# Optimization experiments

Measured on AMD Instinct MI355X. Metric: run time of the kernel, lower is better.

## Reference

```python
import jax, jax.numpy as jnp
import numpy as np

THRESH = 1.0
# Control points exactly as in the source (including the [5.0, 1.0] literal).
SRC = np.array([[0.0, 0.0], [0.5, 0.0], [1.0, 0.0],
                [0.0, 0.5], [0.5, 0.5], [1.0, 0.5],
                [0.0, 1.0], [5.0, 1.0], [1.0, 1.0]], dtype=np.float32)


def _u(r):
    # TPS radial basis: r^2 * log(r + 1e-6)
    return r * r * jnp.log(r + 1e-6)


def _pd(a, b):
    # pairwise euclidean distance a:[M,2], b:[N,2] -> [M,N]
    return jnp.sqrt(jnp.sum((a[:, None, :] - b[None, :, :]) ** 2, -1))


def _tps_fit(c, v):
    # Solve TPS system for control points c:[n,2] with target values v:[n].
    # Returns 'reduced' theta of length n+2 (drops theta[0]), as in tps_theta_from_points(reduced=True).
    n = c.shape[0]
    U = _u(_pd(c, c))                                      # [n,n]
    P = jnp.concatenate([jnp.ones((n, 1), c.dtype), c], 1)  # [n,3]
    A = jnp.zeros((n + 3, n + 3), c.dtype)
    A = A.at[:n, :n].set(U).at[:n, n:].set(P).at[n:, :n].set(P.T)
    rhs = jnp.concatenate([v, jnp.zeros((3,), c.dtype)])
    theta = jnp.linalg.solve(A, rhs)
    return theta[1:]


def _tps_z(x, c, theta):
    # Evaluate reduced TPS at points x:[M,2] with control points c:[n,2].
    w, a = theta[:-3], theta[-3:]
    w = jnp.concatenate([-jnp.sum(w, keepdims=True), w])   # recover dropped weight
    b = _u(_pd(x, c)) @ w                                  # [M]
    return a[0] + a[1] * x[:, 0] + a[2] * x[:, 1] + b


def _tps_grid(mv, H, W):
    # mv:[9,2] moving vectors -> warp grid [H,W,2] in [0,1] coords (x in ch 0, y in ch 1)
    src = jnp.asarray(SRC)
    dst = src + mv
    delta = src - dst                                       # = -mv, as in tps_theta_from_points
    th_x = _tps_fit(dst, delta[:, 0])
    th_y = _tps_fit(dst, delta[:, 1])
    ug = jnp.stack(jnp.meshgrid(jnp.linspace(0.0, 1.0, W, dtype=jnp.float32),
                                jnp.linspace(0.0, 1.0, H, dtype=jnp.float32)), -1)  # [H,W,2]
    xf = ug.reshape(-1, 2)
    dx = _tps_z(xf, dst, th_x).reshape(H, W)
    dy = _tps_z(xf, dst, th_y).reshape(H, W)
    return jnp.stack([dx, dy], -1) + ug


def setup_inputs() -> dict:
    key = jax.random.key(0)
    k1, k2 = jax.random.split(key)
    geo_parameters = jax.random.normal(k1, (8, 9, 2), dtype=jnp.float32) * 0.05
    corr_scores = jax.random.uniform(k2, (8, 48, 48, 48, 48), dtype=jnp.float32)
    return {"geo_parameters": geo_parameters, "corr_scores": corr_scores}


def reference(geo_parameters, corr_scores):
    B = corr_scores.shape[0]
    H, W = corr_scores.shape[-2], corr_scores.shape[-1]
    grids = jax.vmap(lambda mv: _tps_grid(mv, H, W))(geo_parameters)  # [B,H,W,2]
    # Faithful to source: grid * (height-1, width-1) scales channel 0 (x) by H-1, channel 1 (y) by W-1.
    gx = grids[..., 0] * (H - 1)
    gy = grids[..., 1] * (W - 1)
    ax = jnp.arange(W, dtype=gx.dtype)
    ay = jnp.arange(H, dtype=gy.dtype)
    # integer ax in [ceil(gx-t), floor(gx+t)] (clipped to valid range) <=> |ax-gx| <= t
    cx = jnp.abs(ax[None, :, None, None] - gx[:, None, :, :]) <= THRESH  # [B,W_a,H_b,W_b]
    cy = jnp.abs(ay[None, :, None, None] - gy[:, None, :, :]) <= THRESH  # [B,H_a,H_b,W_b]
    mask = (cy[:, :, None, :, :] & cx[:, None, :, :, :]).astype(corr_scores.dtype)  # [B,H,W,H,W]
    inlier_matching = corr_scores * mask
    return inlier_matching, jnp.sum(inlier_matching, axis=(1, 2, 3, 4))
```

## Files before the change

kernel.cpp:

```cpp
#include <hip/hip_runtime.h>

#define HW 48
#define GRID_PER_B (HW * HW)
#define CORR_PER_B (HW * HW * HW * HW)

typedef float f32x4 __attribute__((ext_vector_type(4)));

__global__ __launch_bounds__(256) void tps_grid_kernel(
    const float* __restrict__ geo,
    const float* __restrict__ corr,
    float2* __restrict__ gxy,
    float* __restrict__ sums)
{
    const int b   = blockIdx.x;
    const int tid = threadIdx.x;

    __shared__ double sA[12][14];
    __shared__ double sdx[9], sdy[9];
    __shared__ double s_fac[12];
    __shared__ double s_pinv;
    __shared__ int    s_piv;
    __shared__ float  s_wx[9], s_wy[9], s_ax[3], s_ay[3], s_px[9], s_py[9];
    __shared__ float  s_part[4];

    if (tid < 9) {
        float mvx = geo[(b * 9 + tid) * 2 + 0];
        float mvy = geo[(b * 9 + tid) * 2 + 1];
        const float srcx[9] = {0.f, 0.5f, 1.f, 0.f, 0.5f, 1.f, 0.f, 5.f, 1.f};
        const float srcy[9] = {0.f, 0.f,  0.f, 0.5f,0.5f, 0.5f,1.f, 1.f, 1.f};
        sdx[tid] = (double)srcx[tid] + (double)mvx;
        sdy[tid] = (double)srcy[tid] + (double)mvy;
        sA[tid][12] = -(double)mvx;
        sA[tid][13] = -(double)mvy;
    }
    __syncthreads();
    if (tid < 81) {
        int r = tid / 9, c = tid % 9;
        double dx = sdx[r] - sdx[c];
        double dy = sdy[r] - sdy[c];
        double rr = sqrt(dx * dx + dy * dy);
        sA[r][c] = rr * rr * log(rr + 1e-6);
    } else if (tid < 90) {
        int k = tid - 81;
        sA[k][9]  = 1.0; sA[k][10] = sdx[k]; sA[k][11] = sdy[k];
        sA[9][k]  = 1.0; sA[10][k] = sdx[k]; sA[11][k] = sdy[k];
    } else if (tid < 105) {
        int t = tid - 90;
        sA[9 + t / 5][9 + t % 5] = 0.0;
    }
    __syncthreads();

    for (int col = 0; col < 12; ++col) {
        if (tid == 0) {
            int piv = col; double best = fabs(sA[col][col]);
            for (int r = col + 1; r < 12; ++r) {
                double v = fabs(sA[r][col]);
                if (v > best) { best = v; piv = r; }
            }
            s_piv = piv;
        }
        __syncthreads();
        int piv = s_piv;
        if (piv != col && tid < 14) {
            double t = sA[col][tid]; sA[col][tid] = sA[piv][tid]; sA[piv][tid] = t;
        }
        __syncthreads();
        if (tid == 0) s_pinv = 1.0 / sA[col][col];
        __syncthreads();
        if (tid < 14) sA[col][tid] *= s_pinv;
        __syncthreads();
        if (tid < 12) s_fac[tid] = sA[tid][col];
        __syncthreads();
        if (tid < 168) {
            int r = tid / 14, c = tid % 14;
            if (r != col) sA[r][c] -= s_fac[r] * sA[col][c];
        }
        __syncthreads();
    }

    if (tid == 0) {
        double swx = 0.0, swy = 0.0;
        for (int k = 1; k < 9; ++k) { swx += sA[k][12]; swy += sA[k][13]; }
        s_wx[0] = (float)(-swx); s_wy[0] = (float)(-swy);
        for (int k = 1; k < 9; ++k) {
            s_wx[k] = (float)sA[k][12];
            s_wy[k] = (float)sA[k][13];
        }
        s_ax[0] = (float)sA[9][12];  s_ax[1] = (float)sA[10][12]; s_ax[2] = (float)sA[11][12];
        s_ay[0] = (float)sA[9][13];  s_ay[1] = (float)sA[10][13]; s_ay[2] = (float)sA[11][13];
        for (int k = 0; k < 9; ++k) { s_px[k] = (float)sdx[k]; s_py[k] = (float)sdy[k]; }
    }
    __syncthreads();

    const float* corr_b = corr + (size_t)b * CORR_PER_B;
    float lsum = 0.0f;
    for (int p = tid; p < GRID_PER_B; p += 256) {
        int h = p / HW, w = p % HW;
        float x = (float)w * (1.0f / 47.0f);
        float y = (float)h * (1.0f / 47.0f);
        float zx = s_ax[0] + s_ax[1] * x + s_ax[2] * y;
        float zy = s_ay[0] + s_ay[1] * x + s_ay[2] * y;
        #pragma unroll
        for (int k = 0; k < 9; ++k) {
            float ddx = x - s_px[k], ddy = y - s_py[k];
            float r2 = ddx * ddx + ddy * ddy;
            float u  = r2 * logf(sqrtf(r2) + 1e-6f);
            zx += s_wx[k] * u;
            zy += s_wy[k] * u;
        }
        float gx = (zx + x) * 47.0f;
        float gy = (zy + y) * 47.0f;
        gxy[b * GRID_PER_B + p] = make_float2(gx, gy);

        int ifl = (int)floorf(gx);
        int jfl = (int)floorf(gy);
        for (int dj = -1; dj <= 2; ++dj) {
            int j = jfl + dj;
            if (j < 0 || j > 47) continue;
            if (fabsf((float)j - gy) > 1.0f) continue;
            for (int di = -1; di <= 2; ++di) {
                int i = ifl + di;
                if (i < 0 || i > 47) continue;
                if (fabsf((float)i - gx) > 1.0f) continue;
                lsum += corr_b[(j * HW + i) * GRID_PER_B + p];
            }
        }
    }
    for (int off = 32; off > 0; off >>= 1)
        lsum += __shfl_down(lsum, off, 64);
    const int lane = tid & 63, wv = tid >> 6;
    if (lane == 0) s_part[wv] = lsum;
    __syncthreads();
    if (tid == 0) sums[b] = s_part[0] + s_part[1] + s_part[2] + s_part[3];
}

__global__ __launch_bounds__(256) void mask_apply_kernel(
    const float* __restrict__ corr,
    const float2* __restrict__ gxy,
    float* __restrict__ out)
{
    const int e = (blockIdx.x * 256 + threadIdx.x) * 8;

    int w  = e % 48;
    int t1 = e / 48;
    int h  = t1 % 48;
    int t2 = t1 / 48;
    int i  = t2 % 48;
    int t3 = t2 / 48;
    int j  = t3 % 48;
    int b  = t3 / 48;

    const float fi = (float)i, fj = (float)j;
    const f32x4* g4 = reinterpret_cast<const f32x4*>(gxy + (b * GRID_PER_B + h * HW + w));
    f32x4 ga = g4[0], gb = g4[1], gc = g4[2], gd = g4[3];

    float gx[8] = {ga.x, ga.z, gb.x, gb.z, gc.x, gc.z, gd.x, gd.z};
    float gy[8] = {ga.y, ga.w, gb.y, gb.w, gc.y, gc.w, gd.y, gd.w};

    float v[8];
    #pragma unroll
    for (int c = 0; c < 8; ++c) {
        bool cond = (fabsf(fi - gx[c]) <= 1.0f) && (fabsf(fj - gy[c]) <= 1.0f);
        v[c] = 0.0f;
        if (cond) v[c] = corr[e + c];
    }
    f32x4* o = reinterpret_cast<f32x4*>(out + e);
    f32x4 lo = {v[0], v[1], v[2], v[3]};
    f32x4 hi = {v[4], v[5], v[6], v[7]};
    __builtin_nontemporal_store(lo, o);
    __builtin_nontemporal_store(hi, o + 1);
}

extern "C" void kernel_launch(void* const* d_in, const int* in_sizes, int n_in,
                              void* d_out, int out_size, void* d_ws, size_t ws_size,
                              hipStream_t stream)
{
    const float* geo  = (const float*)d_in[0];
    const float* corr = (const float*)d_in[1];

    const int B = in_sizes[0] / 18;
    const int N = in_sizes[1];

    float*  out  = (float*)d_out;
    float*  sums = out + N;
    float2* gxy  = (float2*)d_ws;

    hipLaunchKernelGGL(tps_grid_kernel, dim3(B), dim3(256), 0, stream,
                       geo, corr, gxy, sums);

    const int nblocks = N / (256 * 8);
    hipLaunchKernelGGL(mask_apply_kernel, dim3(nblocks), dim3(256), 0, stream,
                       corr, gxy, out);
}
```

Baseline: 339.9 us.

## Fuse per-batch sum into mask kernel via wave partials and reduce pass

The per-batch inlier sum moves out of the serial TPS grid kernel, which used only 8 blocks to gather scattered corr values, and into the mask-apply kernel. Each wave there writes a partial sum to workspace, and a small third kernel reduces the partials per batch. Each thread now handles 4 elements instead of 8, so the mask kernel launches twice as many threads. The cost is a third launch, the partial-sum traffic, and a longer dependency chain of kernels.

```diff
diff --git a/kernel.cpp b/kernel.cpp
--- a/kernel.cpp
+++ b/kernel.cpp
@@ -8,9 +8,7 @@
 
 __global__ __launch_bounds__(256) void tps_grid_kernel(
     const float* __restrict__ geo,
-    const float* __restrict__ corr,
-    float2* __restrict__ gxy,
-    float* __restrict__ sums)
+    float2* __restrict__ gxy)
 {
     const int b   = blockIdx.x;
     const int tid = threadIdx.x;
@@ -21,7 +19,6 @@
     __shared__ double s_pinv;
     __shared__ int    s_piv;
     __shared__ float  s_wx[9], s_wy[9], s_ax[3], s_ay[3], s_px[9], s_py[9];
-    __shared__ float  s_part[4];
 
     if (tid < 9) {
         float mvx = geo[(b * 9 + tid) * 2 + 0];
@@ -92,8 +89,6 @@
     }
     __syncthreads();
 
-    const float* corr_b = corr + (size_t)b * CORR_PER_B;
-    float lsum = 0.0f;
     for (int p = tid; p < GRID_PER_B; p += 256) {
         int h = p / HW, w = p % HW;
         float x = (float)w * (1.0f / 47.0f);
@@ -108,38 +103,18 @@
             zx += s_wx[k] * u;
             zy += s_wy[k] * u;
         }
-        float gx = (zx + x) * 47.0f;
-        float gy = (zy + y) * 47.0f;
-        gxy[b * GRID_PER_B + p] = make_float2(gx, gy);
-
-        int ifl = (int)floorf(gx);
-        int jfl = (int)floorf(gy);
-        for (int dj = -1; dj <= 2; ++dj) {
-            int j = jfl + dj;
-            if (j < 0 || j > 47) continue;
-            if (fabsf((float)j - gy) > 1.0f) continue;
-            for (int di = -1; di <= 2; ++di) {
-                int i = ifl + di;
-                if (i < 0 || i > 47) continue;
-                if (fabsf((float)i - gx) > 1.0f) continue;
-                lsum += corr_b[(j * HW + i) * GRID_PER_B + p];
-            }
-        }
+        gxy[b * GRID_PER_B + p] = make_float2((zx + x) * 47.0f, (zy + y) * 47.0f);
     }
-    for (int off = 32; off > 0; off >>= 1)
-        lsum += __shfl_down(lsum, off, 64);
-    const int lane = tid & 63, wv = tid >> 6;
-    if (lane == 0) s_part[wv] = lsum;
-    __syncthreads();
-    if (tid == 0) sums[b] = s_part[0] + s_part[1] + s_part[2] + s_part[3];
 }
 
 __global__ __launch_bounds__(256) void mask_apply_kernel(
     const float* __restrict__ corr,
     const float2* __restrict__ gxy,
-    float* __restrict__ out)
+    float* __restrict__ out,
+    float* __restrict__ partials)
 {
-    const int e = (blockIdx.x * 256 + threadIdx.x) * 8;
+    const int t = blockIdx.x * 256 + threadIdx.x;
+    const int e = t * 4;
 
     int w  = e % 48;
     int t1 = e / 48;
@@ -152,23 +127,48 @@
 
     const float fi = (float)i, fj = (float)j;
     const f32x4* g4 = reinterpret_cast<const f32x4*>(gxy + (b * GRID_PER_B + h * HW + w));
-    f32x4 ga = g4[0], gb = g4[1], gc = g4[2], gd = g4[3];
+    f32x4 g01 = g4[0], g23 = g4[1];
 
-    float gx[8] = {ga.x, ga.z, gb.x, gb.z, gc.x, gc.z, gd.x, gd.z};
-    float gy[8] = {ga.y, ga.w, gb.y, gb.w, gc.y, gc.w, gd.y, gd.w};
+    float gx[4] = {g01.x, g01.z, g23.x, g23.z};
+    float gy[4] = {g01.y, g01.w, g23.y, g23.w};
 
-    float v[8];
+    float v[4];
+    float lsum = 0.0f;
     #pragma unroll
-    for (int c = 0; c < 8; ++c) {
+    for (int c = 0; c < 4; ++c) {
         bool cond = (fabsf(fi - gx[c]) <= 1.0f) && (fabsf(fj - gy[c]) <= 1.0f);
         v[c] = 0.0f;
         if (cond) v[c] = corr[e + c];
+        lsum += v[c];
     }
-    f32x4* o = reinterpret_cast<f32x4*>(out + e);
-    f32x4 lo = {v[0], v[1], v[2], v[3]};
-    f32x4 hi = {v[4], v[5], v[6], v[7]};
-    __builtin_nontemporal_store(lo, o);
-    __builtin_nontemporal_store(hi, o + 1);
+    f32x4 val = {v[0], v[1], v[2], v[3]};
+    __builtin_nontemporal_store(val, reinterpret_cast<f32x4*>(out + e));
+
+    for (int off = 32; off > 0; off >>= 1)
+        lsum += __shfl_down(lsum, off, 64);
+    if ((threadIdx.x & 63) == 0)
+        partials[t >> 6] = lsum;
+}
+
+__global__ __launch_bounds__(256) void reduce_kernel(
+    const float* __restrict__ partials,
+    float* __restrict__ sums,
+    int waves_per_b)
+{
+    const int b   = blockIdx.x;
+    const int tid = threadIdx.x;
+    __shared__ float s_part[4];
+
+    float s = 0.0f;
+    for (int k = tid; k < waves_per_b; k += 256)
+        s += partials[b * waves_per_b + k];
+
+    for (int off = 32; off > 0; off >>= 1)
+        s += __shfl_down(s, off, 64);
+    const int lane = tid & 63, wv = tid >> 6;
+    if (lane == 0) s_part[wv] = s;
+    __syncthreads();
+    if (tid == 0) sums[b] = s_part[0] + s_part[1] + s_part[2] + s_part[3];
 }
 
 extern "C" void kernel_launch(void* const* d_in, const int* in_sizes, int n_in,
@@ -181,14 +181,19 @@
     const int B = in_sizes[0] / 18;
     const int N = in_sizes[1];
 
-    float*  out  = (float*)d_out;
-    float*  sums = out + N;
-    float2* gxy  = (float2*)d_ws;
+    float*  out      = (float*)d_out;
+    float*  sums     = out + N;
+    float2* gxy      = (float2*)d_ws;
+    float*  partials = (float*)d_ws + 2 * B * GRID_PER_B;
 
     hipLaunchKernelGGL(tps_grid_kernel, dim3(B), dim3(256), 0, stream,
-                       geo, corr, gxy, sums);
+                       geo, gxy);
 
-    const int nblocks = N / (256 * 8);
+    const int nblocks = N / (256 * 4);
     hipLaunchKernelGGL(mask_apply_kernel, dim3(nblocks), dim3(256), 0, stream,
-                       corr, gxy, out);
+                       corr, gxy, out, partials);
+
+    const int waves_per_b = (N / B) / 256;
+    hipLaunchKernelGGL(reduce_kernel, dim3(B), dim3(256), 0, stream,
+                       partials, sums, waves_per_b);
 }
```

Result: faster. 311.9 us (-8.2%).

## Replace dense mask pass with zero-fill plus sparse scatter of inlier correlations

Applied to the files above, without the earlier changes.

The dense mask kernel read every correlation score and wrote the masked result. It is replaced by a write-only zero fill of the output, followed by a scatter kernel that reads and copies only the few entries within the threshold window of each warped grid point. That kernel also accumulates per-batch sums via atomics, so the TPS kernel no longer does the sparse sum. This removes the full read of the large correlation tensor, at the cost of an extra launch and float atomics that make the sum order nondeterministic.

```diff
diff --git a/kernel.cpp b/kernel.cpp
--- a/kernel.cpp
+++ b/kernel.cpp
@@ -6,11 +6,18 @@
 
 typedef float f32x4 __attribute__((ext_vector_type(4)));
 
+__global__ __launch_bounds__(256) void fill_zero_kernel(
+    f32x4* __restrict__ out4, int n4)
+{
+    const int stride = gridDim.x * 256;
+    const f32x4 z = {0.0f, 0.0f, 0.0f, 0.0f};
+    for (int idx = blockIdx.x * 256 + threadIdx.x; idx < n4; idx += stride)
+        out4[idx] = z;
+}
+
 __global__ __launch_bounds__(256) void tps_grid_kernel(
     const float* __restrict__ geo,
-    const float* __restrict__ corr,
-    float2* __restrict__ gxy,
-    float* __restrict__ sums)
+    float2* __restrict__ gxy)
 {
     const int b   = blockIdx.x;
     const int tid = threadIdx.x;
@@ -21,7 +28,6 @@
     __shared__ double s_pinv;
     __shared__ int    s_piv;
     __shared__ float  s_wx[9], s_wy[9], s_ax[3], s_ay[3], s_px[9], s_py[9];
-    __shared__ float  s_part[4];
 
     if (tid < 9) {
         float mvx = geo[(b * 9 + tid) * 2 + 0];
@@ -92,8 +98,6 @@
     }
     __syncthreads();
 
-    const float* corr_b = corr + (size_t)b * CORR_PER_B;
-    float lsum = 0.0f;
     for (int p = tid; p < GRID_PER_B; p += 256) {
         int h = p / HW, w = p % HW;
         float x = (float)w * (1.0f / 47.0f);
@@ -108,67 +112,52 @@
             zx += s_wx[k] * u;
             zy += s_wy[k] * u;
         }
-        float gx = (zx + x) * 47.0f;
-        float gy = (zy + y) * 47.0f;
-        gxy[b * GRID_PER_B + p] = make_float2(gx, gy);
+        gxy[b * GRID_PER_B + p] = make_float2((zx + x) * 47.0f, (zy + y) * 47.0f);
+    }
+}
 
-        int ifl = (int)floorf(gx);
-        int jfl = (int)floorf(gy);
-        for (int dj = -1; dj <= 2; ++dj) {
-            int j = jfl + dj;
-            if (j < 0 || j > 47) continue;
-            if (fabsf((float)j - gy) > 1.0f) continue;
-            for (int di = -1; di <= 2; ++di) {
-                int i = ifl + di;
-                if (i < 0 || i > 47) continue;
-                if (fabsf((float)i - gx) > 1.0f) continue;
-                lsum += corr_b[(j * HW + i) * GRID_PER_B + p];
-            }
+__global__ __launch_bounds__(256) void scatter_sum_kernel(
+    const float* __restrict__ corr,
+    const float2* __restrict__ gxy,
+    float* __restrict__ out,
+    float* __restrict__ sums)
+{
+    const int b   = blockIdx.x;
+    const int tid = threadIdx.x;
+    const int p   = blockIdx.y * 256 + tid;
+
+    float2 g = gxy[b * GRID_PER_B + p];
+    const float* corr_b = corr + (size_t)b * CORR_PER_B;
+    float*       out_b  = out  + (size_t)b * CORR_PER_B;
+
+    const int ifl = (int)floorf(g.x);
+    const int jfl = (int)floorf(g.y);
+
+    float lsum = 0.0f;
+    #pragma unroll
+    for (int dj = -1; dj <= 1; ++dj) {
+        int j = jfl + dj;
+        if (j < 0 || j > 47) continue;
+        if (fabsf((float)j - g.y) > 1.0f) continue;
+        #pragma unroll
+        for (int di = -1; di <= 1; ++di) {
+            int i = ifl + di;
+            if (i < 0 || i > 47) continue;
+            if (fabsf((float)i - g.x) > 1.0f) continue;
+            int ofs = (j * HW + i) * GRID_PER_B + p;
+            float v = corr_b[ofs];
+            out_b[ofs] = v;
+            lsum += v;
         }
     }
+
     for (int off = 32; off > 0; off >>= 1)
         lsum += __shfl_down(lsum, off, 64);
-    const int lane = tid & 63, wv = tid >> 6;
-    if (lane == 0) s_part[wv] = lsum;
+    __shared__ float parts[4];
+    if ((tid & 63) == 0) parts[tid >> 6] = lsum;
     __syncthreads();
-    if (tid == 0) sums[b] = s_part[0] + s_part[1] + s_part[2] + s_part[3];
-}
-
-__global__ __launch_bounds__(256) void mask_apply_kernel(
-    const float* __restrict__ corr,
-    const float2* __restrict__ gxy,
-    float* __restrict__ out)
-{
-    const int e = (blockIdx.x * 256 + threadIdx.x) * 8;
-
-    int w  = e % 48;
-    int t1 = e / 48;
-    int h  = t1 % 48;
-    int t2 = t1 / 48;
-    int i  = t2 % 48;
-    int t3 = t2 / 48;
-    int j  = t3 % 48;
-    int b  = t3 / 48;
-
-    const float fi = (float)i, fj = (float)j;
-    const f32x4* g4 = reinterpret_cast<const f32x4*>(gxy + (b * GRID_PER_B + h * HW + w));
-    f32x4 ga = g4[0], gb = g4[1], gc = g4[2], gd = g4[3];
-
-    float gx[8] = {ga.x, ga.z, gb.x, gb.z, gc.x, gc.z, gd.x, gd.z};
-    float gy[8] = {ga.y, ga.w, gb.y, gb.w, gc.y, gc.w, gd.y, gd.w};
-
-    float v[8];
-    #pragma unroll
-    for (int c = 0; c < 8; ++c) {
-        bool cond = (fabsf(fi - gx[c]) <= 1.0f) && (fabsf(fj - gy[c]) <= 1.0f);
-        v[c] = 0.0f;
-        if (cond) v[c] = corr[e + c];
-    }
-    f32x4* o = reinterpret_cast<f32x4*>(out + e);
-    f32x4 lo = {v[0], v[1], v[2], v[3]};
-    f32x4 hi = {v[4], v[5], v[6], v[7]};
-    __builtin_nontemporal_store(lo, o);
-    __builtin_nontemporal_store(hi, o + 1);
+    if (tid == 0)
+        atomicAdd(&sums[b], parts[0] + parts[1] + parts[2] + parts[3]);
 }
 
 extern "C" void kernel_launch(void* const* d_in, const int* in_sizes, int n_in,
@@ -185,10 +174,13 @@
     float*  sums = out + N;
     float2* gxy  = (float2*)d_ws;
 
+    const int n4 = out_size / 4;
+    hipLaunchKernelGGL(fill_zero_kernel, dim3(2048), dim3(256), 0, stream,
+                       (f32x4*)d_out, n4);
+
     hipLaunchKernelGGL(tps_grid_kernel, dim3(B), dim3(256), 0, stream,
-                       geo, corr, gxy, sums);
+                       geo, gxy);
 
-    const int nblocks = N / (256 * 8);
-    hipLaunchKernelGGL(mask_apply_kernel, dim3(nblocks), dim3(256), 0, stream,
-                       corr, gxy, out);
+    hipLaunchKernelGGL(scatter_sum_kernel, dim3(B, GRID_PER_B / 256), dim3(256),
+                       0, stream, corr, gxy, out, sums);
 }
```

New measurement: 281.6 us. 17.1% less time.
